# Performance work log

Measured on AMD Instinct MI355X. Metric: run time of the kernel, lower is better.

## Reference

```python
import jax, jax.numpy as jnp
import numpy as np

N_NODES = 100000
N_CLASSES = 16
N_UEDGES = 1600000
ITERATIONS = 4
EPS = 1e-12
BETA = 3.0


def setup_inputs() -> dict:
    key = jax.random.key(0)
    k1, k2, k3 = jax.random.split(key, 3)
    # undirected edge endpoints
    s0 = jax.random.randint(k1, (N_UEDGES,), 0, N_NODES)
    d0 = jax.random.randint(k2, (N_UEDGES,), 0, N_NODES)
    # directed edges: e carries message src[e] -> dst[e]; rev[e] is the opposite direction
    src = jnp.concatenate([s0, d0])
    dst = jnp.concatenate([d0, s0])
    ar = jnp.arange(N_UEDGES)
    rev = jnp.concatenate([ar + N_UEDGES, ar])
    # prior: positive, row-normalized (labeled nodes would be peaked; generic positive prior)
    u = jax.random.uniform(k3, (N_NODES, N_CLASSES), minval=0.05, maxval=1.0, dtype=jnp.float32)
    prior = u / jnp.maximum(u.sum(-1, keepdims=True), EPS)
    # log edge potential: log(beta) on the diagonal, 0 off-diagonal (as in __init__)
    log_psi = jnp.log(jnp.float32(BETA)) * jnp.eye(N_CLASSES, dtype=jnp.float32)
    return {"prior": prior, "log_psi": log_psi, "src": src, "dst": dst,
            "rev": rev, "iterations": ITERATIONS}


def reference(prior, log_psi, src, dst, rev, iterations):
    n, k = prior.shape
    psi = jnp.exp(log_psi)  # [k,k]
    e2 = src.shape[0]
    # all messages start uniform (non-edge entries in the original [n,n,k] tensor are never read)
    m = jnp.full((e2, k), 1.0 / k, dtype=prior.dtype)

    def step(m, _):
        log_m = jnp.log(m)
        # S[i] = sum of log incoming messages to node i (product in log-space)
        S = jax.ops.segment_sum(log_m, dst, num_segments=n)  # [n,k]
        # leave-one-out: product over nbrs of src[e] excluding dst[e] == exclude reverse message
        loo = jnp.exp(S[src] - log_m[rev])  # [E2,k]
        b = jnp.maximum(prior[src] * loo, EPS)
        m_new = b @ psi
        m_new = m_new / jnp.maximum(m_new.sum(-1, keepdims=True), EPS)
        return m_new, None

    m, _ = jax.lax.scan(step, m, None, length=int(iterations))

    # beliefs: prior * product of all incoming messages, normalized per node
    S = jax.ops.segment_sum(jnp.log(m), dst, num_segments=n)
    b = jnp.maximum(prior * jnp.exp(S), EPS)
    return b / jnp.maximum(b.sum(-1, keepdims=True), EPS)
```

## Files before the change

kernel.cpp:

```cpp
#include <hip/hip_runtime.h>
#include <math.h>


#define KC 16
#define EPSF 1e-12f
#define LOG_EPS (-27.631021115928547f)
#define BLOCK 256
#define LMU (-2.7725887222397811f)
#define RANGE_BITS 15
#define RANGE (1 << RANGE_BITS)
#define HW8 (RANGE / 4)
#define BPR 64
#define MW_LDS 4096

struct Args {
  const float* prior;
  const float* log_psi;
  const int* src;
  const int* dst;
  unsigned int* histos;
  int* deg;
  float* corr;
  int* gcnt;
  unsigned int* actmask;
  int* elist;
  int* alist;
  float* out;
  int n, nk, e2, nr;
};

__device__ __forceinline__ void psi_consts(const float* __restrict__ log_psi,
                                           float* __restrict__ cm1, float& thr) {
#pragma unroll
  for (int c = 0; c < KC; c++) cm1[c] = __expf(log_psi[c * (KC + 1)]) - 1.0f;
  float cmax = cm1[0], cmin = cm1[0];
#pragma unroll
  for (int c = 1; c < KC; c++) { cmax = fmaxf(cmax, cm1[c]); cmin = fminf(cmin, cm1[c]); }
  thr = (cmin >= 0.f && cmax == cmin) ? (LOG_EPS - __logf(16.f + cmax) - 1e-3f)
                                      : -3.0e38f;
}

__device__ __forceinline__ void g_h(const float* __restrict__ Ta,
                                    const float* __restrict__ prev,
                                    const float* __restrict__ cm1,
                                    float* __restrict__ out) {
  float b[KC], t = 0.f;
#pragma unroll
  for (int c = 0; c < KC; c++) {
    float e = fmaxf(__expf(Ta[c] - prev[c]), EPSF);
    b[c] = e; t += e;
  }
  float vs = 0.f;
#pragma unroll
  for (int c = 0; c < KC; c++) {
    float v = fmaf(cm1[c], b[c], t);
    out[c] = v; vs += v;
  }
  float ls = __logf(fmaxf(vs, EPSF));
#pragma unroll
  for (int c = 0; c < KC; c++) out[c] = __logf(out[c]) - ls;
}

template <int S>
__device__ bool msg_rec(int a, int b, const Args& A, const float* __restrict__ cm1,
                        float thr, int ds, float* __restrict__ out) {
  int dgi = A.deg[a];
  if (dgi > ds) {
#pragma unroll
    for (int c = 0; c < KC; c++) out[c] = LMU;
    return false;
  }
  float Ta[KC];
  const float* pr = A.prior + (size_t)a * KC;
  float dg = (float)dgi;
  float mx = -3.0e38f;
  if constexpr (S >= 2) {
    float* co = A.corr + (size_t)(S - 2) * A.nk + (size_t)a * KC;
#pragma unroll
    for (int c = 0; c < KC; c++) {
      float cv = __hip_atomic_load(co + c, __ATOMIC_RELAXED, __HIP_MEMORY_SCOPE_AGENT);
      float t = fmaf(LMU, dg, __logf(pr[c])) + cv;
      Ta[c] = t; mx = fmaxf(mx, t);
    }
  } else {
#pragma unroll
    for (int c = 0; c < KC; c++) {
      float t = fmaf(LMU, dg, __logf(pr[c]));
      Ta[c] = t; mx = fmaxf(mx, t);
    }
  }
  if (mx < thr) {
#pragma unroll
    for (int c = 0; c < KC; c++) out[c] = LMU;
    return false;
  }
  float prev[KC];
  if constexpr (S == 1) {
#pragma unroll
    for (int c = 0; c < KC; c++) prev[c] = LMU;
  } else {
    msg_rec<S - 1>(b, a, A, cm1, thr, ds, prev);
  }
  g_h(Ta, prev, cm1, out);
  return true;
}

__global__ void __launch_bounds__(BLOCK) hist_kernel(Args A) {
  __shared__ unsigned int h[HW8];
  const int tid = threadIdx.x, job = blockIdx.x;
  const int r = job >> 6, bi = job & (BPR - 1);
  for (int k = tid; k < HW8; k += BLOCK) h[k] = 0u;
  __syncthreads();
  const int lo = r << RANGE_BITS;
  const int nv = A.e2 >> 2;
  const int4* d4 = (const int4*)A.dst;
  for (int v = bi * BLOCK + tid; v < nv; v += BPR * BLOCK) {
    int4 x = d4[v];
    int a;
    a = x.x - lo; if ((unsigned)a < RANGE) atomicAdd(&h[a >> 2], 1u << ((a & 3) << 3));
    a = x.y - lo; if ((unsigned)a < RANGE) atomicAdd(&h[a >> 2], 1u << ((a & 3) << 3));
    a = x.z - lo; if ((unsigned)a < RANGE) atomicAdd(&h[a >> 2], 1u << ((a & 3) << 3));
    a = x.w - lo; if ((unsigned)a < RANGE) atomicAdd(&h[a >> 2], 1u << ((a & 3) << 3));
  }
  if (bi == 0) {
    for (int e = (nv << 2) + tid; e < A.e2; e += BLOCK) {
      int a = A.dst[e] - lo;
      if ((unsigned)a < RANGE) atomicAdd(&h[a >> 2], 1u << ((a & 3) << 3));
    }
  }
  __syncthreads();
  unsigned int* o = A.histos + (size_t)job * HW8;
  for (int k = tid; k < HW8; k += BLOCK) o[k] = h[k];

  {
    const int nw = (A.n + 31) >> 5;
    const int stride = (int)gridDim.x * BLOCK;
    for (int k = job * BLOCK + tid; k < nw; k += stride) A.actmask[k] = 0u;
  }
  if (job == 0 && tid == 0) {
    float cm1[KC], thr2;
    psi_consts(A.log_psi, cm1, thr2);
    float cmax = cm1[0], cmin = cm1[0];
#pragma unroll
    for (int c = 1; c < KC; c++) { cmax = fmaxf(cmax, cm1[c]); cmin = fminf(cmin, cm1[c]); }
    int ds = 0x7fffffff, dsb = 0x7fffffff;
    if (cmin >= 0.f && cmax == cmin) {
      float t = LOG_EPS - __logf(16.f + cmax) - 1e-3f;
      float denom = LMU + log1pf(cmax);
      if (denom < 0.f) {
        ds  = (int)floorf(t / denom);
        dsb = (int)floorf((LOG_EPS - 1e-3f) / denom) + 1;
      }
    }
    A.gcnt[0] = 0;
    A.gcnt[1] = ds;
    A.gcnt[2] = dsb;
    A.gcnt[4] = 0;
  }
}

__global__ void __launch_bounds__(BLOCK) deg_kernel(Args A) {
  int q = blockIdx.x * BLOCK + threadIdx.x;
  int nq = (A.n + 3) >> 2;
  if (q >= nq) return;
  int i0 = q << 2;
  int r = i0 >> RANGE_BITS;
  int word = (i0 & (RANGE - 1)) >> 2;
  const unsigned int* base = A.histos + ((size_t)r * BPR) * HW8 + word;
  unsigned int s = 0;
#pragma unroll 8
  for (int k = 0; k < BPR; k++) s += base[(size_t)k * HW8];
  int dd[4] = { (int)(s & 0xffu), (int)((s >> 8) & 0xffu),
                (int)((s >> 16) & 0xffu), (int)((s >> 24) & 0xffu) };
  int4 dq; dq.x = dd[0]; dq.y = dd[1]; dq.z = dd[2]; dq.w = dd[3];
  ((int4*)A.deg)[q] = dq;
  const int ds  = A.gcnt[1];
  const int dsb = A.gcnt[2];
  float4* o4 = (float4*)A.out;
  unsigned int nib = 0;
#pragma unroll
  for (int t = 0; t < 4; t++) {
    int i = i0 + t;
    if (i >= A.n) break;
    int d = dd[t];
    if (d <= ds) {
      nib |= 1u << t;
      float4 z; z.x = 0.f; z.y = 0.f; z.z = 0.f; z.w = 0.f;
#pragma unroll
      for (int g = 0; g < 4; g++) {
        float4* c4 = (float4*)(A.corr + (size_t)g * A.nk + (size_t)i * KC);
        c4[0] = z; c4[1] = z; c4[2] = z; c4[3] = z;
      }
    }
    if (d >= dsb) {
      float4 u; u.x = 0.0625f; u.y = 0.0625f; u.z = 0.0625f; u.w = 0.0625f;
      o4[i * 4 + 0] = u; o4[i * 4 + 1] = u; o4[i * 4 + 2] = u; o4[i * 4 + 3] = u;
    } else {
      int p = atomicAdd(A.gcnt + 4, 1);
      A.alist[p] = i;
    }
  }
  if (nib) atomicOr(A.actmask + (i0 >> 5), nib << (i0 & 31));
}

__device__ __forceinline__ bool bit_on(const unsigned int* m, int i) {
  return (m[(unsigned)i >> 5] >> (i & 31)) & 1u;
}

__global__ void __launch_bounds__(BLOCK) compact_kernel(Args A) {
  __shared__ unsigned int mask[MW_LDS];
  const int tid = threadIdx.x;
  const int nw = (A.n + 31) >> 5;
  const unsigned int* mp;
  if (nw <= MW_LDS) {
    for (int k = tid; k < nw; k += BLOCK) mask[k] = A.actmask[k];
    __syncthreads();
    mp = mask;
  } else {
    mp = A.actmask;
  }
  const int E = A.e2 >> 1;
  const int nv = E >> 2;
  const int4* s4 = (const int4*)A.src;
  const int4* d4 = (const int4*)A.dst;
  const int stride = (int)gridDim.x * BLOCK;
  for (int v = blockIdx.x * BLOCK + tid; v < nv; v += stride) {
    int4 s = s4[v], d = d4[v];
    int e = v << 2;
    if (bit_on(mp, s.x) && bit_on(mp, d.x)) {
      int p = atomicAdd(A.gcnt, 2); A.elist[p] = e;     A.elist[p + 1] = e + E;
    }
    if (bit_on(mp, s.y) && bit_on(mp, d.y)) {
      int p = atomicAdd(A.gcnt, 2); A.elist[p] = e + 1; A.elist[p + 1] = e + 1 + E;
    }
    if (bit_on(mp, s.z) && bit_on(mp, d.z)) {
      int p = atomicAdd(A.gcnt, 2); A.elist[p] = e + 2; A.elist[p + 1] = e + 2 + E;
    }
    if (bit_on(mp, s.w) && bit_on(mp, d.w)) {
      int p = atomicAdd(A.gcnt, 2); A.elist[p] = e + 3; A.elist[p + 1] = e + 3 + E;
    }
  }
  if (blockIdx.x == 0) {
    for (int e = (nv << 2) + tid; e < E; e += BLOCK) {
      if (bit_on(mp, A.src[e]) && bit_on(mp, A.dst[e])) {
        int p = atomicAdd(A.gcnt, 2); A.elist[p] = e; A.elist[p + 1] = e + E;
      }
    }
    for (int e = 2 * E + tid; e < A.e2; e += BLOCK) {
      if (bit_on(mp, A.src[e]) && bit_on(mp, A.dst[e])) {
        int p = atomicAdd(A.gcnt, 1); A.elist[p] = e;
      }
    }
  }
}

template <int GEN>
__device__ __forceinline__ void gen_pass(const Args& A, const float* __restrict__ cm1,
                                         float thr, int ds, int cnt) {
  float* corrG = A.corr + (size_t)(GEN - 1) * A.nk;
  for (int k = threadIdx.x; k < cnt; k += BLOCK) {
    int e = A.elist[k];
    int j = A.src[e], i = A.dst[e];
    float m[KC];
    if (!msg_rec<GEN>(j, i, A, cm1, thr, ds, m)) continue;
    float* cp = corrG + (size_t)i * KC;
#pragma unroll
    for (int c = 0; c < KC; c++) unsafeAtomicAdd(cp + c, m[c] - LMU);
  }
}

__global__ void __launch_bounds__(BLOCK) gens_kernel(Args A) {
  float cm1[KC], thr;
  psi_consts(A.log_psi, cm1, thr);
  const int ds  = A.gcnt[1];
  const int cnt = A.gcnt[0];
  gen_pass<1>(A, cm1, thr, ds, cnt);
  __threadfence(); __syncthreads();
  gen_pass<2>(A, cm1, thr, ds, cnt);
  __threadfence(); __syncthreads();
  gen_pass<3>(A, cm1, thr, ds, cnt);
  __threadfence(); __syncthreads();
  gen_pass<4>(A, cm1, thr, ds, cnt);
  __threadfence(); __syncthreads();
  const int acnt = A.gcnt[4];
  const float* corr4 = A.corr + 3 * (size_t)A.nk;
  for (int k = threadIdx.x; k < acnt; k += BLOCK) {
    int i = A.alist[k];
    float dg = (float)A.deg[i];
    const float* pr = A.prior + (size_t)i * KC;
    float v[KC];
#pragma unroll
    for (int c = 0; c < KC; c++) {
      float cv = __hip_atomic_load(corr4 + (size_t)i * KC + c,
                                   __ATOMIC_RELAXED, __HIP_MEMORY_SCOPE_AGENT);
      v[c] = fmaxf(__expf(fmaf(LMU, dg, __logf(pr[c])) + cv), EPSF);
    }
    float q0 = (v[0] + v[1]) + (v[2] + v[3]);
    float q1 = (v[4] + v[5]) + (v[6] + v[7]);
    float q2 = (v[8] + v[9]) + (v[10] + v[11]);
    float q3 = (v[12] + v[13]) + (v[14] + v[15]);
    float s = fmaxf((q0 + q1) + (q2 + q3), EPSF);
    float* op = A.out + (size_t)i * KC;
#pragma unroll
    for (int c = 0; c < KC; c++) op[c] = v[c] / s;
  }
}

extern "C" void kernel_launch(void* const* d_in, const int* in_sizes, int n_in,
                              void* d_out, int out_size, void* d_ws, size_t ws_size,
                              hipStream_t stream) {
  Args A;
  A.prior   = (const float*)d_in[0];
  A.log_psi = (const float*)d_in[1];
  A.src     = (const int*)d_in[2];
  A.dst     = (const int*)d_in[3];

  int e2 = in_sizes[2];
  int n  = in_sizes[0] / KC;
  A.n = n; A.nk = n * KC; A.e2 = e2;
  A.nr = (n + RANGE - 1) >> RANGE_BITS;

  char* ws = (char*)d_ws;
  size_t off = 0;
  auto alloc = [&](size_t bytes) -> void* {
    void* p = ws + off;
    off = (off + bytes + 255) & ~(size_t)255;
    return p;
  };
  A.histos  = (unsigned int*)alloc((size_t)A.nr * BPR * HW8 * 4);
  A.deg     = (int*)alloc(((size_t)n + 16) * sizeof(int));
  A.corr    = (float*)alloc((size_t)4 * A.nk * sizeof(float));
  A.gcnt    = (int*)alloc(256);
  A.actmask = (unsigned int*)alloc((((size_t)n + 31) / 32 + 128) * 4);
  A.elist   = (int*)alloc((size_t)e2 * sizeof(int));
  A.alist   = (int*)alloc(((size_t)n + 16) * sizeof(int));
  A.out     = (float*)d_out;

  const int gHist = A.nr * BPR;
  const int gDeg  = (((n + 3) >> 2) + BLOCK - 1) / BLOCK;
  hist_kernel<<<gHist, BLOCK, 0, stream>>>(A);
  deg_kernel<<<gDeg, BLOCK, 0, stream>>>(A);
  compact_kernel<<<512, BLOCK, 0, stream>>>(A);
  gens_kernel<<<1, BLOCK, 0, stream>>>(A);
}
```

Baseline: 135.2 us.

## Memoize per-generation messages in LDS and widen histogram node range

Adds a memoized generation pass that stores each active edge's message in a double-buffered shared-memory array. Each generation reads the previous generation's reverse message (paired at p^1 in the edge list) instead of recursively recomputing the message chain, used when the active edge list fits in 512 slots. Separately, the histogram kernel now covers twice as many nodes per block range, with twice as many blocks per range. This adds 64KB of LDS to the gens kernel and 64KB of histogram LDS, which may reduce occupancy.

```diff
diff --git a/kernel.cpp b/kernel.cpp
--- a/kernel.cpp
+++ b/kernel.cpp
@@ -7,11 +7,12 @@
 #define LOG_EPS (-27.631021115928547f)
 #define BLOCK 256
 #define LMU (-2.7725887222397811f)
-#define RANGE_BITS 15
+#define RANGE_BITS 16
 #define RANGE (1 << RANGE_BITS)
 #define HW8 (RANGE / 4)
-#define BPR 64
+#define BPR 128
 #define MW_LDS 4096
+#define MSGC 512
 
 struct Args {
   const float* prior;
@@ -108,7 +109,7 @@
 __global__ void __launch_bounds__(BLOCK) hist_kernel(Args A) {
   __shared__ unsigned int h[HW8];
   const int tid = threadIdx.x, job = blockIdx.x;
-  const int r = job >> 6, bi = job & (BPR - 1);
+  const int r = job / BPR, bi = job % BPR;
   for (int k = tid; k < HW8; k += BLOCK) h[k] = 0u;
   __syncthreads();
   const int lo = r << RANGE_BITS;
@@ -254,6 +255,50 @@
   }
 }
 
+template <int S>
+__device__ __forceinline__ void gen_memo(const Args& A, const float* __restrict__ cm1,
+                                         float thr, int cnt,
+                                         float (*__restrict__ wr)[KC],
+                                         const float (*__restrict__ rd)[KC]) {
+  float* corrW = A.corr + (size_t)(S - 1) * A.nk;
+  for (int p = threadIdx.x; p < cnt; p += BLOCK) {
+    int e = A.elist[p];
+    int j = A.src[e], i = A.dst[e];
+    const float* pr = A.prior + (size_t)j * KC;
+    float dg = (float)A.deg[j];
+    float T[KC], mx = -3.0e38f;
+#pragma unroll
+    for (int c = 0; c < KC; c++) {
+      float t = fmaf(LMU, dg, __logf(pr[c]));
+      if constexpr (S >= 2) {
+        t += __hip_atomic_load(A.corr + (size_t)(S - 2) * A.nk + (size_t)j * KC + c,
+                               __ATOMIC_RELAXED, __HIP_MEMORY_SCOPE_AGENT);
+      }
+      T[c] = t; mx = fmaxf(mx, t);
+    }
+    float out[KC];
+    if (mx < thr) {
+#pragma unroll
+      for (int c = 0; c < KC; c++) out[c] = LMU;
+    } else {
+      float prev[KC];
+      if constexpr (S == 1) {
+#pragma unroll
+        for (int c = 0; c < KC; c++) prev[c] = LMU;
+      } else {
+#pragma unroll
+        for (int c = 0; c < KC; c++) prev[c] = rd[p ^ 1][c];
+      }
+      g_h(T, prev, cm1, out);
+      float* cp = corrW + (size_t)i * KC;
+#pragma unroll
+      for (int c = 0; c < KC; c++) unsafeAtomicAdd(cp + c, out[c] - LMU);
+    }
+#pragma unroll
+    for (int c = 0; c < KC; c++) wr[p][c] = out[c];
+  }
+}
+
 template <int GEN>
 __device__ __forceinline__ void gen_pass(const Args& A, const float* __restrict__ cm1,
                                          float thr, int ds, int cnt) {
@@ -270,18 +315,30 @@
 }
 
 __global__ void __launch_bounds__(BLOCK) gens_kernel(Args A) {
+  __shared__ float msg[2][MSGC][KC];
   float cm1[KC], thr;
   psi_consts(A.log_psi, cm1, thr);
   const int ds  = A.gcnt[1];
   const int cnt = A.gcnt[0];
-  gen_pass<1>(A, cm1, thr, ds, cnt);
-  __threadfence(); __syncthreads();
-  gen_pass<2>(A, cm1, thr, ds, cnt);
-  __threadfence(); __syncthreads();
-  gen_pass<3>(A, cm1, thr, ds, cnt);
-  __threadfence(); __syncthreads();
-  gen_pass<4>(A, cm1, thr, ds, cnt);
-  __threadfence(); __syncthreads();
+  if (cnt <= MSGC && (A.e2 & 1) == 0) {
+    gen_memo<1>(A, cm1, thr, cnt, msg[0], (const float(*)[KC])msg[1]);
+    __threadfence(); __syncthreads();
+    gen_memo<2>(A, cm1, thr, cnt, msg[1], (const float(*)[KC])msg[0]);
+    __threadfence(); __syncthreads();
+    gen_memo<3>(A, cm1, thr, cnt, msg[0], (const float(*)[KC])msg[1]);
+    __threadfence(); __syncthreads();
+    gen_memo<4>(A, cm1, thr, cnt, msg[1], (const float(*)[KC])msg[0]);
+    __threadfence(); __syncthreads();
+  } else {
+    gen_pass<1>(A, cm1, thr, ds, cnt);
+    __threadfence(); __syncthreads();
+    gen_pass<2>(A, cm1, thr, ds, cnt);
+    __threadfence(); __syncthreads();
+    gen_pass<3>(A, cm1, thr, ds, cnt);
+    __threadfence(); __syncthreads();
+    gen_pass<4>(A, cm1, thr, ds, cnt);
+    __threadfence(); __syncthreads();
+  }
   const int acnt = A.gcnt[4];
   const float* corr4 = A.corr + 3 * (size_t)A.nk;
   for (int k = threadIdx.x; k < acnt; k += BLOCK) {
```

Result: faster. 128.5 us (-4.9%).
